# Performance work log

Measured on AMD Instinct MI355X. Metric: run time of the kernel, lower is better.

## Reference

```python
import jax, jax.numpy as jnp
import numpy as np

N, E, F0, H = 100000, 3200000, 256, 128
TEMP = 2.0
ALPHA = 0.2  # leaky relu slope
EPS_BN = 1e-5
EPS_LN = 1e-5


def spmm(vals, row, col, X):
    # sparse [N,N] @ dense [N,D] via gather + segment_sum
    return jax.ops.segment_sum(vals[:, None] * X[col], row, num_segments=N)


def batchnorm(h, g, b):
    mu = jnp.mean(h, axis=0, keepdims=True)
    var = jnp.var(h, axis=0, keepdims=True)
    return (h - mu) * jax.lax.rsqrt(var + EPS_BN) * g + b


def layernorm(h, g, b):
    mu = jnp.mean(h, axis=-1, keepdims=True)
    var = jnp.var(h, axis=-1, keepdims=True)
    return (h - mu) * jax.lax.rsqrt(var + EPS_LN) * g + b


def setup_inputs() -> dict:
    key = jax.random.key(0)
    ks = jax.random.split(key, 32)
    x = jax.random.normal(ks[0], (N, F0), dtype=jnp.float32)
    edge_row = jax.random.randint(ks[1], (E,), 0, N)
    edge_col = jax.random.randint(ks[2], (E,), 0, N)
    adj_vals = jax.random.uniform(ks[3], (E,), dtype=jnp.float32) / 32.0  # ~normalized adj
    sf = lambda k, sh: jax.random.normal(k, sh, dtype=jnp.float32) * 0.05
    in_dim = 3 * F0 + 1
    return {
        "x": x, "edge_row": edge_row, "edge_col": edge_col, "adj_vals": adj_vals,
        # LowPassExtractor (GCN)
        "W_gc1": sf(ks[4], (F0, 2 * H)), "b_gc1": jnp.zeros((2 * H,), jnp.float32),
        "bn1_g": jnp.ones((2 * H,), jnp.float32), "bn1_b": jnp.zeros((2 * H,), jnp.float32),
        "W_gc2": sf(ks[5], (2 * H, H)), "b_gc2": jnp.zeros((H,), jnp.float32),
        "bn2_g": jnp.ones((H,), jnp.float32), "bn2_b": jnp.zeros((H,), jnp.float32),
        # Gating
        "Wg1": sf(ks[6], (in_dim, H)), "bg1": jnp.zeros((H,), jnp.float32),
        "ln_g": jnp.ones((H,), jnp.float32), "ln_b": jnp.zeros((H,), jnp.float32),
        "Wg2": sf(ks[7], (H, 2)), "bg2": jnp.zeros((2,), jnp.float32),
        # HighPassExpert
        "Wxp": sf(ks[8], (F0, H)), "bxp": jnp.zeros((H,), jnp.float32),
        "res_scale": jnp.asarray(1.0, jnp.float32),
        "rn_g": jnp.ones((H,), jnp.float32), "rn_b": jnp.zeros((H,), jnp.float32),
        "Wq": sf(ks[9], (H, H)), "Wk": sf(ks[10], (H, H)), "Wv": sf(ks[11], (H, H)),
    }


def reference(x, edge_row, edge_col, adj_vals,
              W_gc1, b_gc1, bn1_g, bn1_b, W_gc2, b_gc2, bn2_g, bn2_b,
              Wg1, bg1, ln_g, ln_b, Wg2, bg2,
              Wxp, bxp, res_scale, rn_g, rn_b, Wq, Wk, Wv):
    # ---- LowPassExtractor: two GCN layers (spmm(adj, xW)+b) with batchnorm+relu
    h1 = jax.nn.relu(batchnorm(spmm(adj_vals, edge_row, edge_col, x @ W_gc1) + b_gc1, bn1_g, bn1_b))
    low = jax.nn.relu(batchnorm(spmm(adj_vals, edge_row, edge_col, h1 @ W_gc2) + b_gc2, bn2_g, bn2_b))

    # ---- Gating: neighborhood stats via spmm
    AX = spmm(adj_vals, edge_row, edge_col, x)
    deg = jax.ops.segment_sum(adj_vals, edge_row, num_segments=N)[:, None]
    x_mean = AX / (deg + 1e-8)
    AX2 = spmm(adj_vals, edge_row, edge_col, x * x)
    var = AX2 / (deg + 1e-8) - x_mean * x_mean
    x_std = jnp.sqrt(jnp.clip(var, 0.0))
    x_cat = jnp.concatenate([x, AX - x, x_std, deg], axis=1)  # [N, 3*F0+1]
    hg = jax.nn.relu(layernorm(x_cat @ Wg1 + bg1, ln_g, ln_b))
    gate = jax.nn.softmax((hg @ Wg2 + bg2) / TEMP, axis=1)  # [N, 2]

    # ---- HighPassExpert: GAT-style sparse attention on normalized residual
    residual = layernorm(res_scale * (x @ Wxp + bxp - low), rn_g, rn_b)
    Q, K, V = residual @ Wq, residual @ Wk, residual @ Wv
    scores = jnp.sum(Q[edge_row] * K[edge_col], axis=1) / jnp.sqrt(jnp.float32(H))
    exp_s = jnp.exp(jnp.where(scores > 0, scores, ALPHA * scores))
    denom = jax.ops.segment_sum(exp_s, edge_row, num_segments=N)
    attn = exp_s / (denom[edge_row] + 1e-16)
    high = jax.ops.segment_sum(attn[:, None] * V[edge_col], edge_row, num_segments=N)

    output = gate[:, 0:1] * low + gate[:, 1:2] * high
    return output, gate, low, high
```

## Files before the change

### kernel.cpp

```cpp
#include <hip/hip_runtime.h>

#define F0 256
#define HD 128
#define NP 100352

typedef unsigned short u16;
typedef __attribute__((ext_vector_type(8))) short short8;
typedef __attribute__((ext_vector_type(4))) float f32x4;

__device__ inline float bf2f(u16 u) {
    union { unsigned int i; float f; } v; v.i = ((unsigned int)u) << 16; return v.f;
}
__device__ inline u16 f2bf(float f) {
    union { float f; unsigned int i; } v; v.f = f;
    unsigned int r = v.i + 0x7FFF + ((v.i >> 16) & 1);
    return (u16)(r >> 16);
}

__device__ inline float rsum16(float v) {
    v += __shfl_xor(v, 1); v += __shfl_xor(v, 2);
    v += __shfl_xor(v, 4); v += __shfl_xor(v, 8);
    return v;
}

#define GLOAD16(gp, lp) __builtin_amdgcn_global_load_lds( \
    (const __attribute__((address_space(1))) void*)(gp), \
    (__attribute__((address_space(3))) void*)(lp), 16, 0, 0)

__global__ void k_hist_rank(const int* __restrict__ row, int* __restrict__ counts,
                            int* __restrict__ rank, int E) {
    int e = blockIdx.x * blockDim.x + threadIdx.x;
    if (e < E) rank[e] = atomicAdd(&counts[row[e]], 1);
}

__global__ void k_scan_blk(const int* __restrict__ counts, int* __restrict__ scan_out,
                           int* __restrict__ partials, int n) {
    __shared__ int wsum[16];
    int t = threadIdx.x;
    int i = blockIdx.x * 1024 + t;
    int v = (i < n) ? counts[i] : 0;
    int lane = t & 63, w = t >> 6;
    #pragma unroll
    for (int off = 1; off < 64; off <<= 1) { int u = __shfl_up(v, off); if (lane >= off) v += u; }
    if (lane == 63) wsum[w] = v;
    __syncthreads();
    if (t < 16) {
        int s = wsum[t];
        #pragma unroll
        for (int off = 1; off < 16; off <<= 1) { int u = __shfl_up(s, off); if (t >= off) s += u; }
        wsum[t] = s;
    }
    __syncthreads();
    int add = (w > 0) ? wsum[w - 1] : 0;
    if (i < n) scan_out[i] = v + add;
    if (t == 1023) partials[blockIdx.x] = wsum[15];
}

__global__ void k_scan_part(int* partials, int nb) {
    __shared__ int ws2[2];
    int t = threadIdx.x;
    int v = (t < nb) ? partials[t] : 0;
    int lane = t & 63, w = t >> 6;
    #pragma unroll
    for (int off = 1; off < 64; off <<= 1) { int u = __shfl_up(v, off); if (lane >= off) v += u; }
    if (lane == 63) ws2[w] = v;
    __syncthreads();
    if (w == 1) v += ws2[0];
    if (t < nb) partials[t] = v;
}

__global__ void k_scan_add(int* __restrict__ row_ptr, const int* __restrict__ partials, int n) {
    int b = blockIdx.x;
    int i = b * 1024 + threadIdx.x;
    if (b == 0 && threadIdx.x == 0) row_ptr[0] = 0;
    int add = (b > 0) ? partials[b - 1] : 0;
    if (i < n) row_ptr[1 + i] += add;
}

__global__ void k_scatter_direct(const int* __restrict__ row, const int* __restrict__ ecol,
                                 const float* __restrict__ avals, const int* __restrict__ rank,
                                 const int* __restrict__ row_ptr, int2* __restrict__ cv, int E) {
    int e = blockIdx.x * blockDim.x + threadIdx.x;
    if (e >= E) return;
    int r = row[e];
    int pos = row_ptr[r] + rank[e];
    cv[pos] = make_int2(ecol[e], __float_as_int(avals[e]));
}

__global__ void k_cast_x(const float* __restrict__ x, u16* __restrict__ xb, int total4) {
    int i = blockIdx.x * blockDim.x + threadIdx.x;
    if (i >= total4) return;
    float4 v = ((const float4*)x)[i];
    ((ushort4*)xb)[i] = make_ushort4(f2bf(v.x), f2bf(v.y), f2bf(v.z), f2bf(v.w));
}

__global__ void k_prep_w(const float* __restrict__ W_gc1, const float* __restrict__ W_gc2,
                         const float* __restrict__ Wg1, const float* __restrict__ Wxp,
                         const float* __restrict__ Wq, const float* __restrict__ Wk,
                         const float* __restrict__ Wv,
                         u16* Wgc1t, u16* Wgc2t, u16* Wdt, u16* W1t, u16* W2t,
                         u16* Wxpt, u16* Wqt, u16* Wkt, u16* Wvt) {
    int z = blockIdx.z;
    int idx = blockIdx.x * 256 + threadIdx.x;
    if (z == 0) { if (idx < 65536) { int n = idx >> 8, k = idx & 255; Wgc1t[idx] = f2bf(W_gc1[k * 256 + n]); } }
    else if (z == 1) { if (idx < 32768) { int n = idx >> 8, k = idx & 255; Wgc2t[idx] = f2bf(W_gc2[k * 128 + n]); } }
    else if (z == 2) { if (idx < 32768) { int n = idx >> 8, k = idx & 255; Wdt[idx] = f2bf(Wg1[k * 128 + n] - Wg1[(k + 256) * 128 + n]); } }
    else if (z == 3) { if (idx < 32768) { int n = idx >> 8, k = idx & 255; W1t[idx] = f2bf(Wg1[(k + 256) * 128 + n]); } }
    else if (z == 4) { if (idx < 32768) { int n = idx >> 8, k = idx & 255; W2t[idx] = f2bf(Wg1[(k + 512) * 128 + n]); } }
    else if (z == 5) { if (idx < 32768) { int n = idx >> 8, k = idx & 255; Wxpt[idx] = f2bf(Wxp[k * 128 + n]); } }
    else if (z == 6) { if (idx < 16384) { int n = idx >> 7, k = idx & 127; Wqt[idx] = f2bf(Wq[k * 128 + n]); } }
    else if (z == 7) { if (idx < 16384) { int n = idx >> 7, k = idx & 127; Wkt[idx] = f2bf(Wk[k * 128 + n]); } }
    else if (z == 8) { if (idx < 16384) { int n = idx >> 7, k = idx & 127; Wvt[idx] = f2bf(Wv[k * 128 + n]); } }
}

__global__ void k_spmm_x2(const u16* __restrict__ Xb, const int* __restrict__ row_ptr,
                          const int2* __restrict__ cv,
                          u16* __restrict__ AXb, u16* __restrict__ XSTDb,
                          float* __restrict__ deg, int N) {
    int wid = blockIdx.x * 4 + (threadIdx.x >> 6);
    if (wid >= N) return;
    int lane = threadIdx.x & 63;
    float a0 = 0, a1 = 0, a2 = 0, a3 = 0;
    float q0 = 0, q1 = 0, q2 = 0, q3 = 0, d = 0;
    int s = row_ptr[wid], e = row_ptr[wid + 1];
    int j = s;
    for (; j + 7 < e; j += 8) {
        int2 cc[8]; ushort4 xb[8];
        #pragma unroll
        for (int t = 0; t < 8; ++t) cc[t] = cv[j + t];
        #pragma unroll
        for (int t = 0; t < 8; ++t) xb[t] = *(const ushort4*)(Xb + (size_t)cc[t].x * F0 + lane * 4);
        #pragma unroll
        for (int t = 0; t < 8; ++t) {
            float x0 = bf2f(xb[t].x), x1 = bf2f(xb[t].y), x2 = bf2f(xb[t].z), x3 = bf2f(xb[t].w);
            float vv = __int_as_float(cc[t].y);
            a0 += vv * x0; a1 += vv * x1; a2 += vv * x2; a3 += vv * x3;
            q0 += vv * x0 * x0; q1 += vv * x1 * x1; q2 += vv * x2 * x2; q3 += vv * x3 * x3;
            d += vv;
        }
    }
    for (; j + 3 < e; j += 4) {
        int2 cc[4]; ushort4 xb[4];
        #pragma unroll
        for (int t = 0; t < 4; ++t) cc[t] = cv[j + t];
        #pragma unroll
        for (int t = 0; t < 4; ++t) xb[t] = *(const ushort4*)(Xb + (size_t)cc[t].x * F0 + lane * 4);
        #pragma unroll
        for (int t = 0; t < 4; ++t) {
            float x0 = bf2f(xb[t].x), x1 = bf2f(xb[t].y), x2 = bf2f(xb[t].z), x3 = bf2f(xb[t].w);
            float vv = __int_as_float(cc[t].y);
            a0 += vv * x0; a1 += vv * x1; a2 += vv * x2; a3 += vv * x3;
            q0 += vv * x0 * x0; q1 += vv * x1 * x1; q2 += vv * x2 * x2; q3 += vv * x3 * x3;
            d += vv;
        }
    }
    for (; j < e; ++j) {
        int2 cc = cv[j];
        float v0 = __int_as_float(cc.y);
        ushort4 xb0 = *(const ushort4*)(Xb + (size_t)cc.x * F0 + lane * 4);
        float x0 = bf2f(xb0.x), x1 = bf2f(xb0.y), x2 = bf2f(xb0.z), x3 = bf2f(xb0.w);
        a0 += v0 * x0; a1 += v0 * x1; a2 += v0 * x2; a3 += v0 * x3;
        q0 += v0 * x0 * x0; q1 += v0 * x1 * x1; q2 += v0 * x2 * x2; q3 += v0 * x3 * x3;
        d += v0;
    }
    float inv = 1.0f / (d + 1e-8f);
    float m0 = a0 * inv, m1 = a1 * inv, m2 = a2 * inv, m3 = a3 * inv;
    float s0 = sqrtf(fmaxf(q0 * inv - m0 * m0, 0.f));
    float s1 = sqrtf(fmaxf(q1 * inv - m1 * m1, 0.f));
    float s2 = sqrtf(fmaxf(q2 * inv - m2 * m2, 0.f));
    float s3 = sqrtf(fmaxf(q3 * inv - m3 * m3, 0.f));
    *(ushort4*)(AXb + (size_t)wid * F0 + lane * 4) = make_ushort4(f2bf(a0), f2bf(a1), f2bf(a2), f2bf(a3));
    *(ushort4*)(XSTDb + (size_t)wid * F0 + lane * 4) = make_ushort4(f2bf(s0), f2bf(s1), f2bf(s2), f2bf(s3));
    if (lane == 0) deg[wid] = d;
}

__global__ void k_spmm128(const u16* __restrict__ Xb, const int* __restrict__ row_ptr,
                          const int2* __restrict__ cv, u16* __restrict__ OUT, int N) {
    int wid = blockIdx.x * 4 + (threadIdx.x >> 6);
    if (wid >= N) return;
    int lane = threadIdx.x & 63;
    float a0 = 0, a1 = 0;
    int s = row_ptr[wid], e = row_ptr[wid + 1];
    int j = s;
    for (; j + 7 < e; j += 8) {
        int2 cc[8]; ushort2 xb[8];
        #pragma unroll
        for (int t = 0; t < 8; ++t) cc[t] = cv[j + t];
        #pragma unroll
        for (int t = 0; t < 8; ++t) xb[t] = *(const ushort2*)(Xb + (size_t)cc[t].x * HD + lane * 2);
        #pragma unroll
        for (int t = 0; t < 8; ++t) {
            float vv = __int_as_float(cc[t].y);
            a0 += vv * bf2f(xb[t].x); a1 += vv * bf2f(xb[t].y);
        }
    }
    for (; j + 3 < e; j += 4) {
        int2 cc[4]; ushort2 xb[4];
        #pragma unroll
        for (int t = 0; t < 4; ++t) cc[t] = cv[j + t];
        #pragma unroll
        for (int t = 0; t < 4; ++t) xb[t] = *(const ushort2*)(Xb + (size_t)cc[t].x * HD + lane * 2);
        #pragma unroll
        for (int t = 0; t < 4; ++t) {
            float vv = __int_as_float(cc[t].y);
            a0 += vv * bf2f(xb[t].x); a1 += vv * bf2f(xb[t].y);
        }
    }
    for (; j < e; ++j) {
        int2 cc = cv[j];
        float v0 = __int_as_float(cc.y);
        ushort2 x0 = *(const ushort2*)(Xb + (size_t)cc.x * HD + lane * 2);
        a0 += v0 * bf2f(x0.x); a1 += v0 * bf2f(x0.y);
    }
    *(ushort2*)(OUT + (size_t)wid * HD + lane * 2) = make_ushort2(f2bf(a0), f2bf(a1));
}

__device__ inline void mm_core(const u16* __restrict__ A, const u16* __restrict__ Bt,
                               int K, int ldA, int ldB, int m0, int n0,
                               u16* As, u16* Bs, f32x4 acc[4][4]) {
    int t = threadIdx.x, w = t >> 6, l = t & 63;
    int wr = (w >> 1) * 64, wc = (w & 1) * 64;
    int aoff = (wr + (l & 15)) * 32 + (l >> 4) * 8;
    int boff = (wc + (l & 15)) * 32 + (l >> 4) * 8;
    for (int k0 = 0; k0 < K; k0 += 32) {
        __syncthreads();
        #pragma unroll
        for (int s = 0; s < 2; ++s) {
            int i = s * 256 + t;
            int row = i >> 2, ch = i & 3;
            GLOAD16(A + (size_t)(m0 + row) * ldA + k0 + ch * 8, As + i * 8);
            GLOAD16(Bt + (size_t)(n0 + row) * ldB + k0 + ch * 8, Bs + i * 8);
        }
        __syncthreads();
        short8 af[4], bfr[4];
        #pragma unroll
        for (int i = 0; i < 4; ++i) af[i] = *(const short8*)(As + aoff + i * 16 * 32);
        #pragma unroll
        for (int j = 0; j < 4; ++j) bfr[j] = *(const short8*)(Bs + boff + j * 16 * 32);
        #pragma unroll
        for (int i = 0; i < 4; ++i)
            #pragma unroll
            for (int j = 0; j < 4; ++j)
                acc[i][j] = __builtin_amdgcn_mfma_f32_16x16x32_bf16(af[i], bfr[j], acc[i][j], 0, 0, 0);
    }
}

__device__ inline void mm_zero(f32x4 acc[4][4]) {
    #pragma unroll
    for (int i = 0; i < 4; ++i)
        #pragma unroll
        for (int j = 0; j < 4; ++j)
            acc[i][j] = (f32x4){0.f, 0.f, 0.f, 0.f};
}

__global__ __launch_bounds__(256) void k_mm_bf(const u16* __restrict__ A, const u16* __restrict__ Bt,
                                               u16* __restrict__ C, int M, int K, int Nc) {
    __shared__ __align__(16) u16 As[128 * 32];
    __shared__ __align__(16) u16 Bs[128 * 32];
    int m0 = blockIdx.x * 128, n0 = blockIdx.y * 128;
    f32x4 acc[4][4]; mm_zero(acc);
    mm_core(A, Bt, K, K, K, m0, n0, As, Bs, acc);
    int t = threadIdx.x, w = t >> 6, l = t & 63;
    int rbase = m0 + (w >> 1) * 64 + (l >> 4) * 4;
    int cbase = n0 + (w & 1) * 64 + (l & 15);
    #pragma unroll
    for (int j = 0; j < 4; ++j)
        #pragma unroll
        for (int i = 0; i < 4; ++i)
            #pragma unroll
            for (int r = 0; r < 4; ++r) {
                int row = rbase + i * 16 + r;
                if (row < M) C[(size_t)row * Nc + cbase + j * 16] = f2bf(acc[i][j][r]);
            }
}

__global__ __launch_bounds__(256) void k_mm_gate(const u16* A0, const u16* A1, const u16* A2,
                                                 const u16* B0, const u16* B1, const u16* B2,
                                                 const float* __restrict__ bg1,
                                                 const float* __restrict__ wlast,
                                                 const float* __restrict__ deg,
                                                 const float* __restrict__ ln_g,
                                                 const float* __restrict__ ln_b,
                                                 const float* __restrict__ Wg2,
                                                 const float* __restrict__ bg2,
                                                 float* __restrict__ gate, int M) {
    __shared__ __align__(16) u16 As[128 * 32];
    __shared__ __align__(16) u16 Bs[128 * 32];
    __shared__ float ps1[2][128], ps2[2][128], pt0[2][128], pt1[2][128];
    int m0 = blockIdx.x * 128;
    f32x4 acc[4][4]; mm_zero(acc);
    mm_core(A0, B0, 256, 256, 256, m0, 0, As, Bs, acc);
    mm_core(A1, B1, 256, 256, 256, m0, 0, As, Bs, acc);
    mm_core(A2, B2, 256, 256, 256, m0, 0, As, Bs, acc);
    int t = threadIdx.x, w = t >> 6, l = t & 63;
    int hcol = w & 1;
    int lr0 = (w >> 1) * 64 + (l >> 4) * 4;
    int cbase = hcol * 64 + (l & 15);
    float wl[4], bg[4], lg[4], lb[4], wa[4], wb_[4];
    #pragma unroll
    for (int j = 0; j < 4; ++j) {
        int col = cbase + j * 16;
        wl[j] = wlast[col]; bg[j] = bg1[col];
        lg[j] = ln_g[col];  lb[j] = ln_b[col];
        wa[j] = Wg2[col * 2 + 0]; wb_[j] = Wg2[col * 2 + 1];
    }
    #pragma unroll
    for (int i = 0; i < 4; ++i)
        #pragma unroll
        for (int r = 0; r < 4; ++r) {
            int row = m0 + lr0 + i * 16 + r;
            float dgv = (row < M) ? deg[row] : 0.f;
            float s1 = 0.f, s2 = 0.f;
            #pragma unroll
            for (int j = 0; j < 4; ++j) {
                float h = acc[i][j][r] + bg[j] + dgv * wl[j];
                acc[i][j][r] = h;
                s1 += h; s2 += h * h;
            }
            s1 = rsum16(s1); s2 = rsum16(s2);
            if ((l & 15) == 0) { ps1[hcol][lr0 + i * 16 + r] = s1; ps2[hcol][lr0 + i * 16 + r] = s2; }
        }
    __syncthreads();
    #pragma unroll
    for (int i = 0; i < 4; ++i)
        #pragma unroll
        for (int r = 0; r < 4; ++r) {
            int lr = lr0 + i * 16 + r;
            float s1 = ps1[0][lr] + ps1[1][lr];
            float s2 = ps2[0][lr] + ps2[1][lr];
            float mu = s1 * (1.f / 128.f);
            float var = s2 * (1.f / 128.f) - mu * mu;
            float is = 1.0f / sqrtf(var + 1e-5f);
            float t0 = 0.f, t1 = 0.f;
            #pragma unroll
            for (int j = 0; j < 4; ++j) {
                float y = fmaxf((acc[i][j][r] - mu) * is * lg[j] + lb[j], 0.f);
                t0 += y * wa[j]; t1 += y * wb_[j];
            }
            t0 = rsum16(t0); t1 = rsum16(t1);
            if ((l & 15) == 0) { pt0[hcol][lr] = t0; pt1[hcol][lr] = t1; }
        }
    __syncthreads();
    if (hcol == 0 && (l & 15) == 0) {
        float b20 = bg2[0], b21 = bg2[1];
        #pragma unroll
        for (int i = 0; i < 4; ++i)
            #pragma unroll
            for (int r = 0; r < 4; ++r) {
                int lr = lr0 + i * 16 + r;
                int row = m0 + lr;
                if (row >= M) continue;
                float t0 = (pt0[0][lr] + pt0[1][lr] + b20) * 0.5f;
                float t1 = (pt1[0][lr] + pt1[1][lr] + b21) * 0.5f;
                float m = fmaxf(t0, t1);
                float e0 = __expf(t0 - m), e1 = __expf(t1 - m);
                float inv = 1.0f / (e0 + e1);
                gate[(size_t)row * 2 + 0] = e0 * inv;
                gate[(size_t)row * 2 + 1] = e1 * inv;
            }
    }
}

__global__ __launch_bounds__(256) void k_mm_xp(const u16* __restrict__ A, const u16* __restrict__ Bt,
                                               const float* __restrict__ bias,
                                               const float* __restrict__ low,
                                               const float* __restrict__ g,
                                               const float* __restrict__ b,
                                               const float* __restrict__ rs_ptr,
                                               u16* __restrict__ resid, int M) {
    __shared__ __align__(16) u16 As[128 * 32];
    __shared__ __align__(16) u16 Bs[128 * 32];
    __shared__ float ps1[2][128], ps2[2][128];
    int m0 = blockIdx.x * 128;
    f32x4 acc[4][4]; mm_zero(acc);
    mm_core(A, Bt, 256, 256, 256, m0, 0, As, Bs, acc);
    int t = threadIdx.x, w = t >> 6, l = t & 63;
    int hcol = w & 1;
    int lr0 = (w >> 1) * 64 + (l >> 4) * 4;
    int cbase = hcol * 64 + (l & 15);
    float rs = rs_ptr[0];
    float bx[4], lg[4], lb[4];
    #pragma unroll
    for (int j = 0; j < 4; ++j) {
        int col = cbase + j * 16;
        bx[j] = bias[col]; lg[j] = g[col]; lb[j] = b[col];
    }
    #pragma unroll
    for (int i = 0; i < 4; ++i)
        #pragma unroll
        for (int r = 0; r < 4; ++r) {
            int row = m0 + lr0 + i * 16 + r;
            float s1 = 0.f, s2 = 0.f;
            #pragma unroll
            for (int j = 0; j < 4; ++j) {
                float lv = (row < M) ? low[(size_t)row * 128 + cbase + j * 16] : 0.f;
                float h = rs * (acc[i][j][r] + bx[j] - lv);
                acc[i][j][r] = h;
                s1 += h; s2 += h * h;
            }
            s1 = rsum16(s1); s2 = rsum16(s2);
            if ((l & 15) == 0) { ps1[hcol][lr0 + i * 16 + r] = s1; ps2[hcol][lr0 + i * 16 + r] = s2; }
        }
    __syncthreads();
    #pragma unroll
    for (int i = 0; i < 4; ++i)
        #pragma unroll
        for (int r = 0; r < 4; ++r) {
            int lr = lr0 + i * 16 + r;
            int row = m0 + lr;
            float s1 = ps1[0][lr] + ps1[1][lr];
            float s2 = ps2[0][lr] + ps2[1][lr];
            float mu = s1 * (1.f / 128.f);
            float var = s2 * (1.f / 128.f) - mu * mu;
            float is = 1.0f / sqrtf(var + 1e-5f);
            if (row < M) {
                #pragma unroll
                for (int j = 0; j < 4; ++j) {
                    float y = (acc[i][j][r] - mu) * is * lg[j] + lb[j];
                    resid[(size_t)row * 128 + cbase + j * 16] = f2bf(y);
                }
            }
        }
}

__global__ __launch_bounds__(256) void k_mm_qkv(const u16* __restrict__ A,
                                                const u16* Wqt, const u16* Wkt, const u16* Wvt,
                                                u16* Qb, u16* KV, int M) {
    __shared__ __align__(16) u16 As[128 * 32];
    __shared__ __align__(16) u16 Bs[128 * 32];
    int z = blockIdx.z;
    const u16* Bt = (z == 0) ? Wqt : (z == 1) ? Wkt : Wvt;
    int m0 = blockIdx.x * 128;
    f32x4 acc[4][4]; mm_zero(acc);
    mm_core(A, Bt, 128, 128, 128, m0, 0, As, Bs, acc);
    int t = threadIdx.x, w = t >> 6, l = t & 63;
    int rbase = m0 + (w >> 1) * 64 + (l >> 4) * 4;
    int cbase = (w & 1) * 64 + (l & 15);
    if (z == 0) {
        #pragma unroll
        for (int j = 0; j < 4; ++j)
            #pragma unroll
            for (int i = 0; i < 4; ++i)
                #pragma unroll
                for (int r = 0; r < 4; ++r) {
                    int row = rbase + i * 16 + r;
                    if (row < M) Qb[(size_t)row * 128 + cbase + j * 16] = f2bf(acc[i][j][r]);
                }
    } else {
        int coff = (z == 1) ? 0 : 128;
        #pragma unroll
        for (int j = 0; j < 4; ++j)
            #pragma unroll
            for (int i = 0; i < 4; ++i)
                #pragma unroll
                for (int r = 0; r < 4; ++r) {
                    int row = rbase + i * 16 + r;
                    if (row < M) KV[(size_t)row * 256 + coff + cbase + j * 16] = f2bf(acc[i][j][r]);
                }
    }
}

__global__ void k_bn_stats_bf(const u16* __restrict__ H, double* __restrict__ stats, int N, int C) {
    int t = threadIdx.x;
    int rpt = 256 / C;
    int rsub = t / C;
    int col = t - rsub * C;
    double s = 0.0, q = 0.0;
    for (long r = (long)blockIdx.x * rpt + rsub; r < N; r += (long)gridDim.x * rpt) {
        float v = bf2f(H[(size_t)r * C + col]);
        s += v; q += (double)v * v;
    }
    __shared__ double sh_s[256], sh_q[256];
    sh_s[t] = s; sh_q[t] = q;
    __syncthreads();
    if (t < C) {
        for (int k = 1; k < rpt; ++k) { s += sh_s[t + k * C]; q += sh_q[t + k * C]; }
        atomicAdd(&stats[t], s);
        atomicAdd(&stats[C + t], q);
    }
}

__global__ void k_bn_fin(const double* __restrict__ stats, const float* __restrict__ g,
                         const float* __restrict__ b, float* __restrict__ scale,
                         float* __restrict__ shift, int C, double invN) {
    int t = threadIdx.x;
    if (t >= C) return;
    double mean = stats[t] * invN;
    double var = stats[C + t] * invN - mean * mean;
    float sc = (float)((double)g[t] / sqrt(var + 1e-5));
    scale[t] = sc;
    shift[t] = b[t] - (float)mean * sc;
}

__global__ void k_bn_relu_bb(const u16* __restrict__ in, u16* __restrict__ out,
                             const float* __restrict__ scale, const float* __restrict__ shift,
                             int total4, int cmask4) {
    int i = blockIdx.x * blockDim.x + threadIdx.x;
    if (i >= total4) return;
    int c4 = i & cmask4;
    ushort4 v = ((const ushort4*)in)[i];
    float4 sc = ((const float4*)scale)[c4];
    float4 sh = ((const float4*)shift)[c4];
    ((ushort4*)out)[i] = make_ushort4(
        f2bf(fmaxf(bf2f(v.x) * sc.x + sh.x, 0.f)), f2bf(fmaxf(bf2f(v.y) * sc.y + sh.y, 0.f)),
        f2bf(fmaxf(bf2f(v.z) * sc.z + sh.z, 0.f)), f2bf(fmaxf(bf2f(v.w) * sc.w + sh.w, 0.f)));
}

__global__ void k_bn_relu_bf(const u16* __restrict__ in, float* __restrict__ out,
                             const float* __restrict__ scale, const float* __restrict__ shift,
                             int total4, int cmask4) {
    int i = blockIdx.x * blockDim.x + threadIdx.x;
    if (i >= total4) return;
    int c4 = i & cmask4;
    ushort4 v = ((const ushort4*)in)[i];
    float4 sc = ((const float4*)scale)[c4];
    float4 sh = ((const float4*)shift)[c4];
    ((float4*)out)[i] = make_float4(
        fmaxf(bf2f(v.x) * sc.x + sh.x, 0.f), fmaxf(bf2f(v.y) * sc.y + sh.y, 0.f),
        fmaxf(bf2f(v.z) * sc.z + sh.z, 0.f), fmaxf(bf2f(v.w) * sc.w + sh.w, 0.f));
}

__global__ void k_attn_aggr(const u16* __restrict__ Qb, const u16* __restrict__ KV,
                            const int* __restrict__ row_ptr, const int2* __restrict__ cv,
                            const float* __restrict__ gate, const float* __restrict__ low,
                            float* __restrict__ high, float* __restrict__ outp, int N) {
    int wid = blockIdx.x * 4 + (threadIdx.x >> 6);
    if (wid >= N) return;
    int lane = threadIdx.x & 63;
    int sub = lane & 15;
    int g = lane >> 4;
    float qs[8];
    {
        short8 q8 = *(const short8*)(Qb + (size_t)wid * HD + sub * 8);
        #pragma unroll
        for (int k = 0; k < 8; ++k) qs[k] = bf2f((u16)q8[k]);
    }
    float2 qv;
    {
        ushort2 qt = *(const ushort2*)(Qb + (size_t)wid * HD + lane * 2);
        qv.x = bf2f(qt.x); qv.y = bf2f(qt.y);
    }
    float n0 = 0, n1 = 0, den = 0;
    int s = row_ptr[wid], e = row_ptr[wid + 1];
    int j = s;
    for (; j + 7 < e; j += 8) {
        int cg0 = cv[j + g].x;
        int cg1 = cv[j + 4 + g].x;
        short8 ka = *(const short8*)(KV + (size_t)cg0 * 256 + sub * 8);
        short8 kb = *(const short8*)(KV + (size_t)cg1 * 256 + sub * 8);
        float p0 = qs[0] * bf2f((u16)ka[0]) + qs[1] * bf2f((u16)ka[1])
                 + qs[2] * bf2f((u16)ka[2]) + qs[3] * bf2f((u16)ka[3])
                 + qs[4] * bf2f((u16)ka[4]) + qs[5] * bf2f((u16)ka[5])
                 + qs[6] * bf2f((u16)ka[6]) + qs[7] * bf2f((u16)ka[7]);
        float p1 = qs[0] * bf2f((u16)kb[0]) + qs[1] * bf2f((u16)kb[1])
                 + qs[2] * bf2f((u16)kb[2]) + qs[3] * bf2f((u16)kb[3])
                 + qs[4] * bf2f((u16)kb[4]) + qs[5] * bf2f((u16)kb[5])
                 + qs[6] * bf2f((u16)kb[6]) + qs[7] * bf2f((u16)kb[7]);
        p0 += __shfl_xor(p0, 1); p1 += __shfl_xor(p1, 1);
        p0 += __shfl_xor(p0, 2); p1 += __shfl_xor(p1, 2);
        p0 += __shfl_xor(p0, 4); p1 += __shfl_xor(p1, 4);
        p0 += __shfl_xor(p0, 8); p1 += __shfl_xor(p1, 8);
        float sc0 = p0 * 0.08838834764831845f;
        float sc1 = p1 * 0.08838834764831845f;
        float ls0 = sc0 > 0.f ? sc0 : 0.2f * sc0;
        float ls1 = sc1 > 0.f ? sc1 : 0.2f * sc1;
        float ex0 = __expf(ls0);
        float ex1 = __expf(ls1);
        float exb[8]; int cb[8];
        #pragma unroll
        for (int t = 0; t < 4; ++t) {
            exb[t]     = __shfl(ex0, t << 4); cb[t]     = __shfl(cg0, t << 4);
            exb[4 + t] = __shfl(ex1, t << 4); cb[4 + t] = __shfl(cg1, t << 4);
        }
        ushort2 vb[8];
        #pragma unroll
        for (int t = 0; t < 8; ++t) vb[t] = *(const ushort2*)(KV + (size_t)cb[t] * 256 + 128 + lane * 2);
        #pragma unroll
        for (int t = 0; t < 8; ++t) {
            n0 += exb[t] * bf2f(vb[t].x);
            n1 += exb[t] * bf2f(vb[t].y);
            den += exb[t];
        }
    }
    for (; j + 3 < e; j += 4) {
        int cg = cv[j + g].x;
        short8 kk = *(const short8*)(KV + (size_t)cg * 256 + sub * 8);
        float p = qs[0] * bf2f((u16)kk[0]) + qs[1] * bf2f((u16)kk[1])
                + qs[2] * bf2f((u16)kk[2]) + qs[3] * bf2f((u16)kk[3])
                + qs[4] * bf2f((u16)kk[4]) + qs[5] * bf2f((u16)kk[5])
                + qs[6] * bf2f((u16)kk[6]) + qs[7] * bf2f((u16)kk[7]);
        p += __shfl_xor(p, 1); p += __shfl_xor(p, 2);
        p += __shfl_xor(p, 4); p += __shfl_xor(p, 8);
        float sc = p * 0.08838834764831845f;
        float ls = sc > 0.f ? sc : 0.2f * sc;
        float ex = __expf(ls);
        float exb[4]; int cb[4];
        #pragma unroll
        for (int t = 0; t < 4; ++t) { exb[t] = __shfl(ex, t << 4); cb[t] = __shfl(cg, t << 4); }
        ushort2 vb[4];
        #pragma unroll
        for (int t = 0; t < 4; ++t) vb[t] = *(const ushort2*)(KV + (size_t)cb[t] * 256 + 128 + lane * 2);
        #pragma unroll
        for (int t = 0; t < 4; ++t) {
            n0 += exb[t] * bf2f(vb[t].x);
            n1 += exb[t] * bf2f(vb[t].y);
            den += exb[t];
        }
    }
    for (; j < e; ++j) {
        int c0 = cv[j].x;
        ushort2 kb0 = *(const ushort2*)(KV + (size_t)c0 * 256 + lane * 2);
        ushort2 vb0 = *(const ushort2*)(KV + (size_t)c0 * 256 + 128 + lane * 2);
        float sc0 = qv.x * bf2f(kb0.x) + qv.y * bf2f(kb0.y);
        #pragma unroll
        for (int off = 32; off > 0; off >>= 1) sc0 += __shfl_xor(sc0, off);
        float p = sc0 * 0.08838834764831845f;
        float ls = p > 0.f ? p : 0.2f * p;
        float ex = __expf(ls);
        n0 += ex * bf2f(vb0.x); n1 += ex * bf2f(vb0.y); den += ex;
    }
    float inv = 1.0f / (den + 1e-16f);
    float h0 = n0 * inv, h1 = n1 * inv;
    *(float2*)(high + (size_t)wid * HD + lane * 2) = make_float2(h0, h1);
    float g0 = gate[(size_t)wid * 2 + 0], g1 = gate[(size_t)wid * 2 + 1];
    float2 lw = *(const float2*)(low + (size_t)wid * HD + lane * 2);
    *(float2*)(outp + (size_t)wid * HD + lane * 2) = make_float2(g0 * lw.x + g1 * h0, g0 * lw.y + g1 * h1);
}

extern "C" void kernel_launch(void* const* d_in, const int* in_sizes, int n_in,
                              void* d_out, int out_size, void* d_ws, size_t ws_size,
                              hipStream_t stream) {
    const float* x      = (const float*)d_in[0];
    const int*   erow   = (const int*)d_in[1];
    const int*   ecol   = (const int*)d_in[2];
    const float* avals  = (const float*)d_in[3];
    const float* W_gc1  = (const float*)d_in[4];
    const float* bn1_g  = (const float*)d_in[6];
    const float* bn1_b  = (const float*)d_in[7];
    const float* W_gc2  = (const float*)d_in[8];
    const float* bn2_g  = (const float*)d_in[10];
    const float* bn2_b  = (const float*)d_in[11];
    const float* Wg1    = (const float*)d_in[12];
    const float* bg1    = (const float*)d_in[13];
    const float* ln_g   = (const float*)d_in[14];
    const float* ln_b   = (const float*)d_in[15];
    const float* Wg2    = (const float*)d_in[16];
    const float* bg2    = (const float*)d_in[17];
    const float* Wxp    = (const float*)d_in[18];
    const float* bxp    = (const float*)d_in[19];
    const float* rscale = (const float*)d_in[20];
    const float* rn_g   = (const float*)d_in[21];
    const float* rn_b   = (const float*)d_in[22];
    const float* Wq     = (const float*)d_in[23];
    const float* Wk     = (const float*)d_in[24];
    const float* Wv     = (const float*)d_in[25];

    const int N = in_sizes[0] / F0;
    const int E = in_sizes[1];

    char* base = (char*)d_ws;
    size_t off = 0;
    auto carve = [&](size_t bytes) -> char* {
        char* p = base + off;
        off += (bytes + 255) & ~(size_t)255;
        return p;
    };
    double* stats  = (double*)carve(4096);
    float* scaleb  = (float*)carve(1024);
    float* shiftb  = (float*)carve(1024);
    int*   partials= (int*)carve(2048);
    u16* Wgc1t = (u16*)carve(65536 * 2);
    u16* Wgc2t = (u16*)carve(32768 * 2);
    u16* Wdt   = (u16*)carve(32768 * 2);
    u16* W1t   = (u16*)carve(32768 * 2);
    u16* W2t   = (u16*)carve(32768 * 2);
    u16* Wxpt  = (u16*)carve(32768 * 2);
    u16* Wqt   = (u16*)carve(16384 * 2);
    u16* Wkt   = (u16*)carve(16384 * 2);
    u16* Wvt   = (u16*)carve(16384 * 2);
    int*   row_ptr = (int*)carve((size_t)(N + 1) * 4);
    int*   cursor  = (int*)carve((size_t)N * 4);
    float* deg     = (float*)carve((size_t)N * 4);
    int2*  cv      = (int2*)carve((size_t)E * 8);
    u16*   x_bf    = (u16*)carve((size_t)NP * F0 * 2);
    u16*   kvb     = (u16*)carve((size_t)NP * 256 * 2);
    u16*   AX_bf   = (u16*)carve((size_t)NP * F0 * 2);
    u16*   XSTD_bf = (u16*)carve((size_t)NP * F0 * 2);
    u16*   h1_bf   = (u16*)carve((size_t)NP * F0 * 2);
    u16*   S2_bf   = (u16*)carve((size_t)NP * HD * 2);
    u16*   G2_bf   = (u16*)carve((size_t)NP * HD * 2);
    float* M3      = (float*)carve((size_t)NP * HD * 4);
    (void)ws_size; (void)n_in; (void)out_size;

    u16*   S1_bf = h1_bf;
    u16*   resid_bf = h1_bf;
    int*   rank  = (int*)M3;
    u16*   Qb    = (u16*)M3;

    float* out_o    = (float*)d_out;
    float* out_gate = out_o + (size_t)N * HD;
    float* out_low  = out_gate + (size_t)N * 2;
    float* out_high = out_low + (size_t)N * HD;

    const int eb  = (E + 255) / 256;
    const int wb  = (N + 3) / 4;
    const int NB1 = (N + 1023) / 1024;
    const int gx  = (N + 127) / 128;
    const dim3 blk(256);

    hipMemsetAsync(cursor, 0, (size_t)N * 4, stream);
    k_hist_rank<<<eb, blk, 0, stream>>>(erow, cursor, rank, E);
    k_scan_blk<<<NB1, 1024, 0, stream>>>(cursor, row_ptr + 1, partials, N);
    k_scan_part<<<1, 128, 0, stream>>>(partials, NB1);
    k_scan_add<<<NB1, 1024, 0, stream>>>(row_ptr, partials, N);
    k_scatter_direct<<<eb, blk, 0, stream>>>(erow, ecol, avals, rank, row_ptr, cv, E);

    k_cast_x<<<(N * 64 + 255) / 256, blk, 0, stream>>>(x, x_bf, N * 64);
    k_prep_w<<<dim3(256, 1, 9), blk, 0, stream>>>(W_gc1, W_gc2, Wg1, Wxp, Wq, Wk, Wv,
                                                  Wgc1t, Wgc2t, Wdt, W1t, W2t, Wxpt, Wqt, Wkt, Wvt);

    k_spmm_x2<<<wb, blk, 0, stream>>>(x_bf, row_ptr, cv, AX_bf, XSTD_bf, deg, N);

    k_mm_bf<<<dim3(gx, 2), blk, 0, stream>>>(AX_bf, Wgc1t, S1_bf, N, 256, 256);
    hipMemsetAsync(stats, 0, 4096, stream);
    k_bn_stats_bf<<<1024, blk, 0, stream>>>(S1_bf, stats, N, 256);
    k_bn_fin<<<1, blk, 0, stream>>>(stats, bn1_g, bn1_b, scaleb, shiftb, 256, 1.0 / N);
    k_bn_relu_bb<<<(N * 64 + 255) / 256, blk, 0, stream>>>(S1_bf, h1_bf, scaleb, shiftb, N * 64, 63);
    k_mm_bf<<<dim3(gx, 1), blk, 0, stream>>>(h1_bf, Wgc2t, G2_bf, N, 256, 128);
    k_spmm128<<<wb, blk, 0, stream>>>(G2_bf, row_ptr, cv, S2_bf, N);
    hipMemsetAsync(stats, 0, 2048, stream);
    k_bn_stats_bf<<<1024, blk, 0, stream>>>(S2_bf, stats, N, 128);
    k_bn_fin<<<1, blk, 0, stream>>>(stats, bn2_g, bn2_b, scaleb, shiftb, 128, 1.0 / N);
    k_bn_relu_bf<<<(N * 32 + 255) / 256, blk, 0, stream>>>(S2_bf, out_low, scaleb, shiftb, N * 32, 31);

    k_mm_gate<<<dim3(gx, 1), blk, 0, stream>>>(x_bf, AX_bf, XSTD_bf, Wdt, W1t, W2t,
                                               bg1, Wg1 + (size_t)768 * 128, deg,
                                               ln_g, ln_b, Wg2, bg2, out_gate, N);

    k_mm_xp<<<dim3(gx, 1), blk, 0, stream>>>(x_bf, Wxpt, bxp, out_low, rn_g, rn_b, rscale,
                                             resid_bf, N);
    k_mm_qkv<<<dim3(gx, 1, 3), blk, 0, stream>>>(resid_bf, Wqt, Wkt, Wvt, Qb, kvb, N);
    k_attn_aggr<<<wb, blk, 0, stream>>>(Qb, kvb, row_ptr, cv, out_gate, out_low, out_high, out_o, N);
}
```

Measured before the change: 1.410 ms.

## Restructure attention V accumulation per edge group and add nontemporal hints

The attention kernel now has each 16-lane group load both the K and V rows of its own edge with 16-byte vector loads and accumulate 8 output features per lane. This replaces broadcasting the exp scores and column indices by shuffle and then issuing narrow V loads, at the cost of a cross-group shuffle reduction at the end. The scalar tail loop becomes a masked 4-wide loop, and the 4-wide middle loops in the spmm kernels are removed. Nontemporal loads and stores are added for the CSR stream, for index arrays in the scatter, and for the output writes, to reduce cache pollution.

```diff
diff --git a/kernel.cpp b/kernel.cpp
--- a/kernel.cpp
+++ b/kernel.cpp
@@ -7,6 +7,8 @@
 typedef unsigned short u16;
 typedef __attribute__((ext_vector_type(8))) short short8;
 typedef __attribute__((ext_vector_type(4))) float f32x4;
+typedef __attribute__((ext_vector_type(4))) unsigned short u16x4;
+typedef __attribute__((ext_vector_type(2))) unsigned short u16x2;
 
 __device__ inline float bf2f(u16 u) {
     union { unsigned int i; float f; } v; v.i = ((unsigned int)u) << 16; return v.f;
@@ -83,8 +85,11 @@
     int e = blockIdx.x * blockDim.x + threadIdx.x;
     if (e >= E) return;
     int r = row[e];
-    int pos = row_ptr[r] + rank[e];
-    cv[pos] = make_int2(ecol[e], __float_as_int(avals[e]));
+    int c = __builtin_nontemporal_load(ecol + e);
+    float v = __builtin_nontemporal_load(avals + e);
+    int rk = __builtin_nontemporal_load(rank + e);
+    int pos = row_ptr[r] + rk;
+    cv[pos] = make_int2(c, __float_as_int(v));
 }
 
 __global__ void k_cast_x(const float* __restrict__ x, u16* __restrict__ xb, int total4) {
@@ -125,39 +130,24 @@
     int s = row_ptr[wid], e = row_ptr[wid + 1];
     int j = s;
     for (; j + 7 < e; j += 8) {
-        int2 cc[8]; ushort4 xb[8];
-        #pragma unroll
-        for (int t = 0; t < 8; ++t) cc[t] = cv[j + t];
-        #pragma unroll
-        for (int t = 0; t < 8; ++t) xb[t] = *(const ushort4*)(Xb + (size_t)cc[t].x * F0 + lane * 4);
+        long long cc[8]; ushort4 xb[8];
+        #pragma unroll
+        for (int t = 0; t < 8; ++t) cc[t] = __builtin_nontemporal_load((const long long*)(cv + j + t));
+        #pragma unroll
+        for (int t = 0; t < 8; ++t) xb[t] = *(const ushort4*)(Xb + (size_t)(int)cc[t] * F0 + lane * 4);
         #pragma unroll
         for (int t = 0; t < 8; ++t) {
             float x0 = bf2f(xb[t].x), x1 = bf2f(xb[t].y), x2 = bf2f(xb[t].z), x3 = bf2f(xb[t].w);
-            float vv = __int_as_float(cc[t].y);
+            float vv = __int_as_float((int)(cc[t] >> 32));
             a0 += vv * x0; a1 += vv * x1; a2 += vv * x2; a3 += vv * x3;
             q0 += vv * x0 * x0; q1 += vv * x1 * x1; q2 += vv * x2 * x2; q3 += vv * x3 * x3;
             d += vv;
         }
     }
-    for (; j + 3 < e; j += 4) {
-        int2 cc[4]; ushort4 xb[4];
-        #pragma unroll
-        for (int t = 0; t < 4; ++t) cc[t] = cv[j + t];
-        #pragma unroll
-        for (int t = 0; t < 4; ++t) xb[t] = *(const ushort4*)(Xb + (size_t)cc[t].x * F0 + lane * 4);
-        #pragma unroll
-        for (int t = 0; t < 4; ++t) {
-            float x0 = bf2f(xb[t].x), x1 = bf2f(xb[t].y), x2 = bf2f(xb[t].z), x3 = bf2f(xb[t].w);
-            float vv = __int_as_float(cc[t].y);
-            a0 += vv * x0; a1 += vv * x1; a2 += vv * x2; a3 += vv * x3;
-            q0 += vv * x0 * x0; q1 += vv * x1 * x1; q2 += vv * x2 * x2; q3 += vv * x3 * x3;
-            d += vv;
-        }
-    }
     for (; j < e; ++j) {
-        int2 cc = cv[j];
-        float v0 = __int_as_float(cc.y);
-        ushort4 xb0 = *(const ushort4*)(Xb + (size_t)cc.x * F0 + lane * 4);
+        long long cc = __builtin_nontemporal_load((const long long*)(cv + j));
+        float v0 = __int_as_float((int)(cc >> 32));
+        ushort4 xb0 = *(const ushort4*)(Xb + (size_t)(int)cc * F0 + lane * 4);
         float x0 = bf2f(xb0.x), x1 = bf2f(xb0.y), x2 = bf2f(xb0.z), x3 = bf2f(xb0.w);
         a0 += v0 * x0; a1 += v0 * x1; a2 += v0 * x2; a3 += v0 * x3;
         q0 += v0 * x0 * x0; q1 += v0 * x1 * x1; q2 += v0 * x2 * x2; q3 += v0 * x3 * x3;
@@ -169,8 +159,10 @@
     float s1 = sqrtf(fmaxf(q1 * inv - m1 * m1, 0.f));
     float s2 = sqrtf(fmaxf(q2 * inv - m2 * m2, 0.f));
     float s3 = sqrtf(fmaxf(q3 * inv - m3 * m3, 0.f));
-    *(ushort4*)(AXb + (size_t)wid * F0 + lane * 4) = make_ushort4(f2bf(a0), f2bf(a1), f2bf(a2), f2bf(a3));
-    *(ushort4*)(XSTDb + (size_t)wid * F0 + lane * 4) = make_ushort4(f2bf(s0), f2bf(s1), f2bf(s2), f2bf(s3));
+    u16x4 axv = {f2bf(a0), f2bf(a1), f2bf(a2), f2bf(a3)};
+    u16x4 sdv = {f2bf(s0), f2bf(s1), f2bf(s2), f2bf(s3)};
+    __builtin_nontemporal_store(axv, (u16x4*)(AXb + (size_t)wid * F0 + lane * 4));
+    __builtin_nontemporal_store(sdv, (u16x4*)(XSTDb + (size_t)wid * F0 + lane * 4));
     if (lane == 0) deg[wid] = d;
 }
 
@@ -183,36 +175,25 @@
     int s = row_ptr[wid], e = row_ptr[wid + 1];
     int j = s;
     for (; j + 7 < e; j += 8) {
-        int2 cc[8]; ushort2 xb[8];
-        #pragma unroll
-        for (int t = 0; t < 8; ++t) cc[t] = cv[j + t];
-        #pragma unroll
-        for (int t = 0; t < 8; ++t) xb[t] = *(const ushort2*)(Xb + (size_t)cc[t].x * HD + lane * 2);
+        long long cc[8]; ushort2 xb[8];
+        #pragma unroll
+        for (int t = 0; t < 8; ++t) cc[t] = __builtin_nontemporal_load((const long long*)(cv + j + t));
+        #pragma unroll
+        for (int t = 0; t < 8; ++t) xb[t] = *(const ushort2*)(Xb + (size_t)(int)cc[t] * HD + lane * 2);
         #pragma unroll
         for (int t = 0; t < 8; ++t) {
-            float vv = __int_as_float(cc[t].y);
+            float vv = __int_as_float((int)(cc[t] >> 32));
             a0 += vv * bf2f(xb[t].x); a1 += vv * bf2f(xb[t].y);
         }
     }
-    for (; j + 3 < e; j += 4) {
-        int2 cc[4]; ushort2 xb[4];
-        #pragma unroll
-        for (int t = 0; t < 4; ++t) cc[t] = cv[j + t];
-        #pragma unroll
-        for (int t = 0; t < 4; ++t) xb[t] = *(const ushort2*)(Xb + (size_t)cc[t].x * HD + lane * 2);
-        #pragma unroll
-        for (int t = 0; t < 4; ++t) {
-            float vv = __int_as_float(cc[t].y);
-            a0 += vv * bf2f(xb[t].x); a1 += vv * bf2f(xb[t].y);
-        }
-    }
     for (; j < e; ++j) {
-        int2 cc = cv[j];
-        float v0 = __int_as_float(cc.y);
-        ushort2 x0 = *(const ushort2*)(Xb + (size_t)cc.x * HD + lane * 2);
+        long long cc = __builtin_nontemporal_load((const long long*)(cv + j));
+        float v0 = __int_as_float((int)(cc >> 32));
+        ushort2 x0 = *(const ushort2*)(Xb + (size_t)(int)cc * HD + lane * 2);
         a0 += v0 * bf2f(x0.x); a1 += v0 * bf2f(x0.y);
     }
-    *(ushort2*)(OUT + (size_t)wid * HD + lane * 2) = make_ushort2(f2bf(a0), f2bf(a1));
+    u16x2 ov = {f2bf(a0), f2bf(a1)};
+    __builtin_nontemporal_store(ov, (u16x2*)(OUT + (size_t)wid * HD + lane * 2));
 }
 
 __device__ inline void mm_core(const u16* __restrict__ A, const u16* __restrict__ Bt,
@@ -535,19 +516,21 @@
         #pragma unroll
         for (int k = 0; k < 8; ++k) qs[k] = bf2f((u16)q8[k]);
     }
-    float2 qv;
-    {
-        ushort2 qt = *(const ushort2*)(Qb + (size_t)wid * HD + lane * 2);
-        qv.x = bf2f(qt.x); qv.y = bf2f(qt.y);
-    }
-    float n0 = 0, n1 = 0, den = 0;
+    float va[8];
+    #pragma unroll
+    for (int k = 0; k < 8; ++k) va[k] = 0.f;
+    float den = 0.f;
     int s = row_ptr[wid], e = row_ptr[wid + 1];
     int j = s;
     for (; j + 7 < e; j += 8) {
-        int cg0 = cv[j + g].x;
-        int cg1 = cv[j + 4 + g].x;
-        short8 ka = *(const short8*)(KV + (size_t)cg0 * 256 + sub * 8);
-        short8 kb = *(const short8*)(KV + (size_t)cg1 * 256 + sub * 8);
+        long long cc0 = __builtin_nontemporal_load((const long long*)(cv + j + g));
+        long long cc1 = __builtin_nontemporal_load((const long long*)(cv + j + 4 + g));
+        const u16* r0 = KV + (size_t)(int)cc0 * 256;
+        const u16* r1 = KV + (size_t)(int)cc1 * 256;
+        short8 ka = *(const short8*)(r0 + sub * 8);
+        short8 kb = *(const short8*)(r1 + sub * 8);
+        short8 wa = *(const short8*)(r0 + 128 + sub * 8);
+        short8 wb = *(const short8*)(r1 + 128 + sub * 8);
         float p0 = qs[0] * bf2f((u16)ka[0]) + qs[1] * bf2f((u16)ka[1])
                  + qs[2] * bf2f((u16)ka[2]) + qs[3] * bf2f((u16)ka[3])
                  + qs[4] * bf2f((u16)ka[4]) + qs[5] * bf2f((u16)ka[5])
@@ -566,25 +549,18 @@
         float ls1 = sc1 > 0.f ? sc1 : 0.2f * sc1;
         float ex0 = __expf(ls0);
         float ex1 = __expf(ls1);
-        float exb[8]; int cb[8];
-        #pragma unroll
-        for (int t = 0; t < 4; ++t) {
-            exb[t]     = __shfl(ex0, t << 4); cb[t]     = __shfl(cg0, t << 4);
-            exb[4 + t] = __shfl(ex1, t << 4); cb[4 + t] = __shfl(cg1, t << 4);
-        }
-        ushort2 vb[8];
-        #pragma unroll
-        for (int t = 0; t < 8; ++t) vb[t] = *(const ushort2*)(KV + (size_t)cb[t] * 256 + 128 + lane * 2);
-        #pragma unroll
-        for (int t = 0; t < 8; ++t) {
-            n0 += exb[t] * bf2f(vb[t].x);
-            n1 += exb[t] * bf2f(vb[t].y);
-            den += exb[t];
-        }
-    }
-    for (; j + 3 < e; j += 4) {
-        int cg = cv[j + g].x;
-        short8 kk = *(const short8*)(KV + (size_t)cg * 256 + sub * 8);
+        #pragma unroll
+        for (int k = 0; k < 8; ++k)
+            va[k] += ex0 * bf2f((u16)wa[k]) + ex1 * bf2f((u16)wb[k]);
+        den += ex0 + ex1;
+    }
+    for (; j < e; j += 4) {
+        int jj = j + g;
+        bool act = jj < e;
+        long long cc = __builtin_nontemporal_load((const long long*)(cv + (act ? jj : j)));
+        const u16* r0 = KV + (size_t)(int)cc * 256;
+        short8 kk = *(const short8*)(r0 + sub * 8);
+        short8 ww = *(const short8*)(r0 + 128 + sub * 8);
         float p = qs[0] * bf2f((u16)kk[0]) + qs[1] * bf2f((u16)kk[1])
                 + qs[2] * bf2f((u16)kk[2]) + qs[3] * bf2f((u16)kk[3])
                 + qs[4] * bf2f((u16)kk[4]) + qs[5] * bf2f((u16)kk[5])
@@ -593,38 +569,34 @@
         p += __shfl_xor(p, 4); p += __shfl_xor(p, 8);
         float sc = p * 0.08838834764831845f;
         float ls = sc > 0.f ? sc : 0.2f * sc;
-        float ex = __expf(ls);
-        float exb[4]; int cb[4];
-        #pragma unroll
-        for (int t = 0; t < 4; ++t) { exb[t] = __shfl(ex, t << 4); cb[t] = __shfl(cg, t << 4); }
-        ushort2 vb[4];
-        #pragma unroll
-        for (int t = 0; t < 4; ++t) vb[t] = *(const ushort2*)(KV + (size_t)cb[t] * 256 + 128 + lane * 2);
-        #pragma unroll
-        for (int t = 0; t < 4; ++t) {
-            n0 += exb[t] * bf2f(vb[t].x);
-            n1 += exb[t] * bf2f(vb[t].y);
-            den += exb[t];
-        }
-    }
-    for (; j < e; ++j) {
-        int c0 = cv[j].x;
-        ushort2 kb0 = *(const ushort2*)(KV + (size_t)c0 * 256 + lane * 2);
-        ushort2 vb0 = *(const ushort2*)(KV + (size_t)c0 * 256 + 128 + lane * 2);
-        float sc0 = qv.x * bf2f(kb0.x) + qv.y * bf2f(kb0.y);
-        #pragma unroll
-        for (int off = 32; off > 0; off >>= 1) sc0 += __shfl_xor(sc0, off);
-        float p = sc0 * 0.08838834764831845f;
-        float ls = p > 0.f ? p : 0.2f * p;
-        float ex = __expf(ls);
-        n0 += ex * bf2f(vb0.x); n1 += ex * bf2f(vb0.y); den += ex;
-    }
-    float inv = 1.0f / (den + 1e-16f);
-    float h0 = n0 * inv, h1 = n1 * inv;
-    *(float2*)(high + (size_t)wid * HD + lane * 2) = make_float2(h0, h1);
-    float g0 = gate[(size_t)wid * 2 + 0], g1 = gate[(size_t)wid * 2 + 1];
-    float2 lw = *(const float2*)(low + (size_t)wid * HD + lane * 2);
-    *(float2*)(outp + (size_t)wid * HD + lane * 2) = make_float2(g0 * lw.x + g1 * h0, g0 * lw.y + g1 * h1);
+        float ex = act ? __expf(ls) : 0.f;
+        #pragma unroll
+        for (int k = 0; k < 8; ++k) va[k] += ex * bf2f((u16)ww[k]);
+        den += ex;
+    }
+    #pragma unroll
+    for (int k = 0; k < 8; ++k) {
+        va[k] += __shfl_xor(va[k], 16);
+        va[k] += __shfl_xor(va[k], 32);
+    }
+    den += __shfl_xor(den, 16);
+    den += __shfl_xor(den, 32);
+    if (g == 0) {
+        float inv = 1.0f / (den + 1e-16f);
+        float g0 = gate[(size_t)wid * 2 + 0], g1 = gate[(size_t)wid * 2 + 1];
+        f32x4 lw0 = __builtin_nontemporal_load((const f32x4*)(low + (size_t)wid * HD + sub * 8));
+        f32x4 lw1 = __builtin_nontemporal_load((const f32x4*)(low + (size_t)wid * HD + sub * 8 + 4));
+        f32x4 h0 = {va[0] * inv, va[1] * inv, va[2] * inv, va[3] * inv};
+        f32x4 h1 = {va[4] * inv, va[5] * inv, va[6] * inv, va[7] * inv};
+        __builtin_nontemporal_store(h0, (f32x4*)(high + (size_t)wid * HD + sub * 8));
+        __builtin_nontemporal_store(h1, (f32x4*)(high + (size_t)wid * HD + sub * 8 + 4));
+        f32x4 o0 = {g0 * lw0[0] + g1 * h0[0], g0 * lw0[1] + g1 * h0[1],
+                    g0 * lw0[2] + g1 * h0[2], g0 * lw0[3] + g1 * h0[3]};
+        f32x4 o1 = {g0 * lw1[0] + g1 * h1[0], g0 * lw1[1] + g1 * h1[1],
+                    g0 * lw1[2] + g1 * h1[2], g0 * lw1[3] + g1 * h1[3]};
+        __builtin_nontemporal_store(o0, (f32x4*)(outp + (size_t)wid * HD + sub * 8));
+        __builtin_nontemporal_store(o1, (f32x4*)(outp + (size_t)wid * HD + sub * 8 + 4));
+    }
 }
 
 extern "C" void kernel_launch(void* const* d_in, const int* in_sizes, int n_in,
```

Result: slower. 1.459 ms (+3.5%).
